# Performance work log

Measured on AMD Instinct MI355X. Metric: run time of the kernel, lower is better.

The kernel has to match this reference:

```python
import jax, jax.numpy as jnp
import numpy as np


def setup_inputs() -> dict:
    key = jax.random.key(0)
    ks = jax.random.split(key, 7)
    T, B, D, H, Q = 256, 128, 1024, 2048, 1024
    return {
        "x": jax.random.normal(ks[0], (T, B, D), dtype=jnp.float32),
        "h0": jax.random.normal(ks[1], (B, H), dtype=jnp.float32) * 0.01,
        "W_xh": jax.random.normal(ks[2], (D, H), dtype=jnp.float32) * 0.01,
        "W_hh": jax.random.normal(ks[3], (H, H), dtype=jnp.float32) * 0.01,
        "b_h": jnp.zeros((H,), dtype=jnp.float32),
        "W_hq": jax.random.normal(ks[4], (H, Q), dtype=jnp.float32) * 0.01,
        "b_q": jnp.zeros((Q,), dtype=jnp.float32),
    }


def reference(x, h0, W_xh, W_hh, b_h, W_hq, b_q):
    # x: (T, B, D); vanilla RNN recurrence with ReLU, per-step output projection.
    def step(h, xt):
        h = jax.nn.relu(xt @ W_xh + h @ W_hh + b_h)  # (B, H)
        return h, h @ W_hq + b_q                      # (B, Q)

    h, outs = jax.lax.scan(step, h0, x)               # outs: (T, B, Q)
    out = outs.reshape(-1, outs.shape[-1])            # torch.cat along dim 0 -> (T*B, Q)
    return out, h
```

## Files before the change

kernel.cpp:

```cpp
#include <hip/hip_runtime.h>
#include <hip/hip_bf16.h>

typedef __bf16 bf16_t;
typedef bf16_t bf16x8 __attribute__((ext_vector_type(8)));
typedef bf16_t bf16x4 __attribute__((ext_vector_type(4)));
typedef bf16_t bf16x2 __attribute__((ext_vector_type(2)));
typedef float f32x4 __attribute__((ext_vector_type(4)));
typedef float f32x2 __attribute__((ext_vector_type(2)));

__device__ __forceinline__ void load_lds16(const bf16_t* g, bf16_t* l) {
  __builtin_amdgcn_global_load_lds(
      (const __attribute__((address_space(1))) unsigned int*)g,
      (__attribute__((address_space(3))) unsigned int*)l,
      16, 0, 0);
}

__global__ void conv_f32_bf16(const float* __restrict__ src,
                              bf16_t* __restrict__ dst, long n) {
  long i = ((long)blockIdx.x * blockDim.x + threadIdx.x) * 8;
  if (i + 7 >= n) return;
  float4 a = *(const float4*)(src + i);
  float4 b = *(const float4*)(src + i + 4);
  bf16x8 v;
  v[0] = (bf16_t)a.x; v[1] = (bf16_t)a.y; v[2] = (bf16_t)a.z; v[3] = (bf16_t)a.w;
  v[4] = (bf16_t)b.x; v[5] = (bf16_t)b.y; v[6] = (bf16_t)b.z; v[7] = (bf16_t)b.w;
  *(bf16x8*)(dst + i) = v;
}

__global__ void conv_bf16_f32(const bf16_t* __restrict__ src,
                              float* __restrict__ dst, long n) {
  long i = (long)blockIdx.x * blockDim.x + threadIdx.x;
  if (i >= n) return;
  dst[i] = (float)src[i];
}

__global__ void transpose_conv(const float* __restrict__ src,
                               bf16_t* __restrict__ dst, int Ksrc, int Nsrc) {
  __shared__ float tile[32][33];
  int n0 = blockIdx.x * 32, k0 = blockIdx.y * 32;
  int tx = threadIdx.x, ty = threadIdx.y;
#pragma unroll
  for (int i = 0; i < 32; i += 8)
    tile[ty + i][tx] = src[(long)(k0 + ty + i) * Nsrc + n0 + tx];
  __syncthreads();
#pragma unroll
  for (int i = 0; i < 32; i += 8)
    dst[(long)(n0 + ty + i) * Ksrc + k0 + tx] = (bf16_t)tile[tx][ty + i];
}

template <int STORE_MODE>
__global__ __launch_bounds__(256) void gemm_bt_128(
    const bf16_t* __restrict__ A, const bf16_t* __restrict__ Bt,
    const float* __restrict__ bias, void* __restrict__ Dout,
    int M, int N, int K) {
  __shared__ bf16_t As[128 * 32];
  __shared__ bf16_t Bs[128 * 32];
  const int tid = threadIdx.x;
  const int lane = tid & 63;
  const int w = tid >> 6;
  const int wr = w >> 1, wc = w & 1;
  const int m0 = blockIdx.y * 128, n0 = blockIdx.x * 128;

  f32x4 acc[4][4] = {};

  const int r0 = tid >> 2;
  const int kk = (tid & 3) * 8;
  const int fr = lane & 15;
  const int fk = (lane >> 4) * 8;

  for (int k0 = 0; k0 < K; k0 += 32) {
    load_lds16(A + (long)(m0 + r0) * K + k0 + kk, As + w * 512);
    load_lds16(A + (long)(m0 + 64 + r0) * K + k0 + kk, As + 2048 + w * 512);
    load_lds16(Bt + (long)(n0 + r0) * K + k0 + kk, Bs + w * 512);
    load_lds16(Bt + (long)(n0 + 64 + r0) * K + k0 + kk, Bs + 2048 + w * 512);
    asm volatile("s_waitcnt vmcnt(0)" ::: "memory");
    __syncthreads();

    bf16x8 af[4], bfx[4];
#pragma unroll
    for (int m = 0; m < 4; ++m)
      af[m] = *(const bf16x8*)&As[(wr * 64 + m * 16 + fr) * 32 + fk];
#pragma unroll
    for (int n = 0; n < 4; ++n)
      bfx[n] = *(const bf16x8*)&Bs[(wc * 64 + n * 16 + fr) * 32 + fk];
#pragma unroll
    for (int m = 0; m < 4; ++m)
#pragma unroll
      for (int n = 0; n < 4; ++n)
        acc[m][n] = __builtin_amdgcn_mfma_f32_16x16x32_bf16(af[m], bfx[n],
                                                            acc[m][n], 0, 0, 0);
    __syncthreads();
  }

  const int fq = lane >> 4;
#pragma unroll
  for (int m = 0; m < 4; ++m) {
#pragma unroll
    for (int n = 0; n < 4; ++n) {
      int col = n0 + wc * 64 + n * 16 + fr;
      float bv = bias[col];
#pragma unroll
      for (int r = 0; r < 4; ++r) {
        int row = m0 + wr * 64 + m * 16 + fq * 4 + r;
        float v = acc[m][n][r] + bv;
        if (STORE_MODE == 0)
          ((float*)Dout)[(long)row * N + col] = v;
        else
          ((bf16_t*)Dout)[(long)row * N + col] = (bf16_t)v;
      }
    }
  }
}

__device__ __forceinline__ void half_bar(unsigned int* c, unsigned int target,
                                         int lane) {
  if (lane == 0)
    __hip_atomic_fetch_add(c, 1u, __ATOMIC_RELEASE,
                           __HIP_MEMORY_SCOPE_WORKGROUP);
  unsigned int v;
  do {
    v = __hip_atomic_load(c, __ATOMIC_ACQUIRE, __HIP_MEMORY_SCOPE_WORKGROUP);
    if (v >= target) break;
    __builtin_amdgcn_s_sleep(1);
  } while (true);
}

__global__ __launch_bounds__(512, 1) void rnn_persistent8(
    const bf16_t* __restrict__ h0,
    bf16_t* __restrict__ Hbuf,
    const bf16_t* __restrict__ WhhT,
    unsigned int* __restrict__ flags) {
  __shared__ bf16_t Wlds[65536];
  __shared__ float sred[2][4][16 * 36];
  __shared__ unsigned int barc[2];

  const int tid = threadIdx.x, lane = tid & 63, w = tid >> 6;
  const int h = w >> 2;
  const int lw = w & 3;
  const int gid = blockIdx.x;
  const int p = (gid >> 1) & 3;
  const int n0idx = ((gid & 1) << 5) | (gid >> 3);
  const int chain = p + h * 4;
  const int m0 = chain * 16, n0 = n0idx * 32;
  const int H = 2048;
  const long BH = 128L * 2048;
  const int kb = lw * 512;
  const int fr = lane & 15, fg = lane >> 4;
  const int w64 = lw * 64;

  {
    const int scol = tid >> 4;
    const int sk16 = tid & 15;
    const bf16_t* gsrc = WhhT + (long)(n0 + scol) * H + sk16 * 8;
#pragma unroll 4
    for (int j = 0; j < 16; ++j) {
      bf16x8 v = *(const bf16x8*)(gsrc + j * 128);
      int k8 = sk16 + j * 16;
      *(bf16x8*)&Wlds[(k8 * 32 + scol) * 8] = v;
    }
  }
  if (tid < 2) barc[tid] = 0;
  __syncthreads();

  const int halftid = tid & 255;
  const int jj = halftid * 2;
  const int zrow = jj >> 5, zcol = jj & 31;
  const int sidx = zrow * 36 + zcol;

  unsigned int* myflag = flags + (((chain << 6) | n0idx) << 4);
  const unsigned int* pollflag =
      flags + (((chain << 6) | (lw * 16 + (lane & 15))) << 4);
  unsigned int* bc = &barc[h];

  for (int t = 0; t < 256; ++t) {
    const bf16_t* hp = (t == 0) ? h0 : Hbuf + (long)(t - 1) * BH;
    bf16_t* z = Hbuf + (long)t * BH;
    const long zoff = (long)(m0 + zrow) * H + n0 + zcol;

    float zvr;
    {
      const bf16_t* zp = z + zoff;
      asm volatile("global_load_dword %0, %1, off sc0 sc1"
                   : "=v"(zvr)
                   : "v"(zp)
                   : "memory");
    }

    if (t > 0) {
      unsigned int v;
      do {
        v = __hip_atomic_load(pollflag, __ATOMIC_RELAXED,
                              __HIP_MEMORY_SCOPE_AGENT);
        if (__all(v >= (unsigned int)t)) break;
        __builtin_amdgcn_s_sleep(1);
      } while (true);
    }

    const bf16_t* Ab = hp + (long)(m0 + fr) * H + kb + fg * 8;
    f32x4 a0, a1, a2, a3, a4, a5, a6, a7, a8, a9, a10, a11, a12, a13, a14, a15;
    asm volatile(
        "global_load_dwordx4 %0, %16, off sc0\n\t"
        "global_load_dwordx4 %1, %16, off offset:64 sc0\n\t"
        "global_load_dwordx4 %2, %16, off offset:128 sc0\n\t"
        "global_load_dwordx4 %3, %16, off offset:192 sc0\n\t"
        "global_load_dwordx4 %4, %16, off offset:256 sc0\n\t"
        "global_load_dwordx4 %5, %16, off offset:320 sc0\n\t"
        "global_load_dwordx4 %6, %16, off offset:384 sc0\n\t"
        "global_load_dwordx4 %7, %16, off offset:448 sc0\n\t"
        "global_load_dwordx4 %8, %16, off offset:512 sc0\n\t"
        "global_load_dwordx4 %9, %16, off offset:576 sc0\n\t"
        "global_load_dwordx4 %10, %16, off offset:640 sc0\n\t"
        "global_load_dwordx4 %11, %16, off offset:704 sc0\n\t"
        "global_load_dwordx4 %12, %16, off offset:768 sc0\n\t"
        "global_load_dwordx4 %13, %16, off offset:832 sc0\n\t"
        "global_load_dwordx4 %14, %16, off offset:896 sc0\n\t"
        "global_load_dwordx4 %15, %16, off offset:960 sc0\n\t"
        "s_waitcnt vmcnt(0)"
        : "=&v"(a0), "=&v"(a1), "=&v"(a2), "=&v"(a3), "=&v"(a4), "=&v"(a5),
          "=&v"(a6), "=&v"(a7), "=&v"(a8), "=&v"(a9), "=&v"(a10), "=&v"(a11),
          "=&v"(a12), "=&v"(a13), "=&v"(a14), "=&v"(a15)
        : "v"(Ab)
        : "memory");
    __builtin_amdgcn_sched_barrier(0);

    f32x4 acc0 = {}, acc1 = {};
#define STEPX(ks, A)                                                          \
  {                                                                           \
    bf16x8 w0 = *(const bf16x8*)&Wlds[((w64 + (ks) * 4 + fg) * 32 + fr) * 8]; \
    bf16x8 w1 =                                                               \
        *(const bf16x8*)&Wlds[((w64 + (ks) * 4 + fg) * 32 + 16 + fr) * 8];    \
    bf16x8 av = __builtin_bit_cast(bf16x8, A);                                \
    acc0 = __builtin_amdgcn_mfma_f32_16x16x32_bf16(av, w0, acc0, 0, 0, 0);    \
    acc1 = __builtin_amdgcn_mfma_f32_16x16x32_bf16(av, w1, acc1, 0, 0, 0);    \
  }
    STEPX(0, a0)   STEPX(1, a1)   STEPX(2, a2)   STEPX(3, a3)
    STEPX(4, a4)   STEPX(5, a5)   STEPX(6, a6)   STEPX(7, a7)
    STEPX(8, a8)   STEPX(9, a9)   STEPX(10, a10) STEPX(11, a11)
    STEPX(12, a12) STEPX(13, a13) STEPX(14, a14) STEPX(15, a15)
#undef STEPX

#pragma unroll
    for (int rr = 0; rr < 4; ++rr) {
      sred[h][lw][(fg * 4 + rr) * 36 + fr] = acc0[rr];
      sred[h][lw][(fg * 4 + rr) * 36 + 16 + fr] = acc1[rr];
    }
    half_bar(bc, (unsigned int)(2 * t + 1) * 4, lane);

    f32x2 r = *(const f32x2*)&sred[h][0][sidx];
    {
      f32x2 r1 = *(const f32x2*)&sred[h][1][sidx];
      f32x2 r2 = *(const f32x2*)&sred[h][2][sidx];
      f32x2 r3 = *(const f32x2*)&sred[h][3][sidx];
      r = r + r1 + r2 + r3;
    }
    bf16x2 zv = __builtin_bit_cast(bf16x2, zvr);
    bf16x2 o;
#pragma unroll
    for (int c2 = 0; c2 < 2; ++c2) {
      float v = r[c2] + (float)zv[c2];
      o[c2] = (bf16_t)(v > 0.f ? v : 0.f);
    }
    const bf16_t* zp = z + zoff;
    {
      float ov = __builtin_bit_cast(float, o);
      asm volatile("global_store_dword %0, %1, off sc0 sc1" ::"v"(zp),
                   "v"(ov)
                   : "memory");
    }
    asm volatile("s_waitcnt vmcnt(0)" ::: "memory");
    half_bar(bc, (unsigned int)(2 * t + 2) * 4, lane);
    if (halftid == 0)
      __hip_atomic_store(myflag, (unsigned int)(t + 1), __ATOMIC_RELAXED,
                         __HIP_MEMORY_SCOPE_AGENT);
    {
      float dummy;
      asm volatile("global_load_dword %0, %1, off sc0"
                   : "=&v"(dummy)
                   : "v"(zp)
                   : "memory");
    }
  }
}

extern "C" void kernel_launch(void* const* d_in, const int* in_sizes, int n_in,
                              void* d_out, int out_size, void* d_ws,
                              size_t ws_size, hipStream_t stream) {
  const float* x   = (const float*)d_in[0];
  const float* h0  = (const float*)d_in[1];
  const float* Wxh = (const float*)d_in[2];
  const float* Whh = (const float*)d_in[3];
  const float* bh  = (const float*)d_in[4];
  const float* Whq = (const float*)d_in[5];
  const float* bq  = (const float*)d_in[6];
  float* out = (float*)d_out;

  const int T = 256, B = 128, D = 1024, H = 2048, Q = 1024;
  const long MB = (long)T * B;

  char* ws = (char*)d_ws;
  unsigned int* flags = (unsigned int*)ws;  ws += 512 * 64;
  bf16_t* x_bf = (bf16_t*)ws;  ws += MB * D * 2;
  bf16_t* Hbuf = (bf16_t*)ws;  ws += MB * H * 2;
  bf16_t* h0bf = (bf16_t*)ws;  ws += (long)B * H * 2;
  bf16_t* WxhT = (bf16_t*)ws;  ws += (long)H * D * 2;
  bf16_t* WhhT = (bf16_t*)ws;  ws += (long)H * H * 2;
  bf16_t* WhqT = (bf16_t*)ws;  ws += (long)Q * H * 2;

  hipMemsetAsync(flags, 0, 512 * 64, stream);

  conv_f32_bf16<<<(int)(MB * D / 8 / 256), 256, 0, stream>>>(x, x_bf, MB * D);
  conv_f32_bf16<<<(int)((long)B * H / 8 / 256), 256, 0, stream>>>(h0, h0bf,
                                                                  (long)B * H);
  transpose_conv<<<dim3(H / 32, D / 32), dim3(32, 8), 0, stream>>>(Wxh, WxhT, D, H);
  transpose_conv<<<dim3(H / 32, H / 32), dim3(32, 8), 0, stream>>>(Whh, WhhT, H, H);
  transpose_conv<<<dim3(Q / 32, H / 32), dim3(32, 8), 0, stream>>>(Whq, WhqT, H, Q);

  gemm_bt_128<1><<<dim3(H / 128, MB / 128), 256, 0, stream>>>(
      x_bf, WxhT, bh, Hbuf, (int)MB, H, D);

  rnn_persistent8<<<256, 512, 0, stream>>>(h0bf, Hbuf, WhhT, flags);

  gemm_bt_128<0><<<dim3(Q / 128, MB / 128), 256, 0, stream>>>(
      Hbuf, WhqT, bq, out, (int)MB, Q, H);

  conv_bf16_f32<<<(int)((long)B * H / 256), 256, 0, stream>>>(
      Hbuf + (long)(T - 1) * B * H, out + MB * Q, (long)B * H);
}
```

Measured before the change: 1.841 ms.

## Cut per-step barriers in persistent RNN kernel; single-wave epilogue with free flag

Replaces the two half-block barriers per timestep with one barrier plus an LDS 'free' flag. One wave per half now does the reduction, ReLU, 16-byte store and global flag publish, so the other waves can start the next step's load and MFMA work without waiting for the epilogue. Also drops the trailing dummy load, staggers the two halves at start, and switches the cross-block poll to an escalating sleep backoff. The backoff may add latency when a dependency arrives just after a long sleep, and putting the whole epilogue on a single wave lengthens that wave's critical path.

```diff
diff --git a/kernel.cpp b/kernel.cpp
--- a/kernel.cpp
+++ b/kernel.cpp
@@ -125,7 +125,7 @@
   } while (true);
 }
 
-__global__ __launch_bounds__(512, 1) void rnn_persistent8(
+__global__ __launch_bounds__(512, 1) void rnn_persistent10(
     const bf16_t* __restrict__ h0,
     bf16_t* __restrict__ Hbuf,
     const bf16_t* __restrict__ WhhT,
@@ -133,6 +133,7 @@
   __shared__ bf16_t Wlds[65536];
   __shared__ float sred[2][4][16 * 36];
   __shared__ unsigned int barc[2];
+  __shared__ unsigned int sfree[2];
 
   const int tid = threadIdx.x, lane = tid & 63, w = tid >> 6;
   const int h = w >> 2;
@@ -159,41 +160,58 @@
       *(bf16x8*)&Wlds[(k8 * 32 + scol) * 8] = v;
     }
   }
-  if (tid < 2) barc[tid] = 0;
+  if (tid < 2) { barc[tid] = 0; sfree[tid] = 0; }
   __syncthreads();
 
-  const int halftid = tid & 255;
-  const int jj = halftid * 2;
-  const int zrow = jj >> 5, zcol = jj & 31;
-  const int sidx = zrow * 36 + zcol;
+  if (h == 1) __builtin_amdgcn_s_sleep(64);
+
+  const int zrowW = lane >> 2, zcolW = (lane & 3) * 8;
+  const int sidx = zrowW * 36 + zcolW;
+  const long zoffW = (long)(m0 + zrowW) * H + n0 + zcolW;
 
   unsigned int* myflag = flags + (((chain << 6) | n0idx) << 4);
   const unsigned int* pollflag =
       flags + (((chain << 6) | (lw * 16 + (lane & 15))) << 4);
   unsigned int* bc = &barc[h];
+  unsigned int* sf = &sfree[h];
 
   for (int t = 0; t < 256; ++t) {
     const bf16_t* hp = (t == 0) ? h0 : Hbuf + (long)(t - 1) * BH;
     bf16_t* z = Hbuf + (long)t * BH;
-    const long zoff = (long)(m0 + zrow) * H + n0 + zcol;
-
-    float zvr;
-    {
-      const bf16_t* zp = z + zoff;
-      asm volatile("global_load_dword %0, %1, off sc0 sc1"
+
+    f32x4 zvr;
+    if (lw == 0) {
+      const bf16_t* zp = z + zoffW;
+      asm volatile("global_load_dwordx4 %0, %1, off sc0 sc1"
                    : "=v"(zvr)
                    : "v"(zp)
                    : "memory");
     }
 
     if (t > 0) {
-      unsigned int v;
-      do {
+      const unsigned int tt = (unsigned int)t;
+      unsigned int v = __hip_atomic_load(pollflag, __ATOMIC_RELAXED,
+                                         __HIP_MEMORY_SCOPE_AGENT);
+      if (!__all(v >= tt)) {
+        __builtin_amdgcn_s_sleep(2);
         v = __hip_atomic_load(pollflag, __ATOMIC_RELAXED,
                               __HIP_MEMORY_SCOPE_AGENT);
-        if (__all(v >= (unsigned int)t)) break;
-        __builtin_amdgcn_s_sleep(1);
-      } while (true);
+        if (!__all(v >= tt)) {
+          __builtin_amdgcn_s_sleep(4);
+          v = __hip_atomic_load(pollflag, __ATOMIC_RELAXED,
+                                __HIP_MEMORY_SCOPE_AGENT);
+          if (!__all(v >= tt)) {
+            __builtin_amdgcn_s_sleep(8);
+            v = __hip_atomic_load(pollflag, __ATOMIC_RELAXED,
+                                  __HIP_MEMORY_SCOPE_AGENT);
+            while (!__all(v >= tt)) {
+              __builtin_amdgcn_s_sleep(16);
+              v = __hip_atomic_load(pollflag, __ATOMIC_RELAXED,
+                                    __HIP_MEMORY_SCOPE_AGENT);
+            }
+          }
+        }
+      }
     }
 
     const bf16_t* Ab = hp + (long)(m0 + fr) * H + kb + fg * 8;
@@ -239,45 +257,51 @@
     STEPX(12, a12) STEPX(13, a13) STEPX(14, a14) STEPX(15, a15)
 #undef STEPX
 
+    if (t > 0) {
+      while (__hip_atomic_load(sf, __ATOMIC_ACQUIRE,
+                               __HIP_MEMORY_SCOPE_WORKGROUP) <
+             (unsigned int)t)
+        __builtin_amdgcn_s_sleep(1);
+    }
+
 #pragma unroll
     for (int rr = 0; rr < 4; ++rr) {
       sred[h][lw][(fg * 4 + rr) * 36 + fr] = acc0[rr];
       sred[h][lw][(fg * 4 + rr) * 36 + 16 + fr] = acc1[rr];
     }
-    half_bar(bc, (unsigned int)(2 * t + 1) * 4, lane);
-
-    f32x2 r = *(const f32x2*)&sred[h][0][sidx];
-    {
-      f32x2 r1 = *(const f32x2*)&sred[h][1][sidx];
-      f32x2 r2 = *(const f32x2*)&sred[h][2][sidx];
-      f32x2 r3 = *(const f32x2*)&sred[h][3][sidx];
-      r = r + r1 + r2 + r3;
-    }
-    bf16x2 zv = __builtin_bit_cast(bf16x2, zvr);
-    bf16x2 o;
-#pragma unroll
-    for (int c2 = 0; c2 < 2; ++c2) {
-      float v = r[c2] + (float)zv[c2];
-      o[c2] = (bf16_t)(v > 0.f ? v : 0.f);
-    }
-    const bf16_t* zp = z + zoff;
-    {
-      float ov = __builtin_bit_cast(float, o);
-      asm volatile("global_store_dword %0, %1, off sc0 sc1" ::"v"(zp),
-                   "v"(ov)
-                   : "memory");
-    }
-    asm volatile("s_waitcnt vmcnt(0)" ::: "memory");
-    half_bar(bc, (unsigned int)(2 * t + 2) * 4, lane);
-    if (halftid == 0)
-      __hip_atomic_store(myflag, (unsigned int)(t + 1), __ATOMIC_RELAXED,
-                         __HIP_MEMORY_SCOPE_AGENT);
-    {
-      float dummy;
-      asm volatile("global_load_dword %0, %1, off sc0"
-                   : "=&v"(dummy)
-                   : "v"(zp)
-                   : "memory");
+    half_bar(bc, (unsigned int)(t + 1) * 4, lane);
+
+    if (lw == 0) {
+      f32x4 slo = *(const f32x4*)&sred[h][0][sidx];
+      f32x4 shi = *(const f32x4*)&sred[h][0][sidx + 4];
+#pragma unroll
+      for (int ww = 1; ww < 4; ++ww) {
+        slo = slo + *(const f32x4*)&sred[h][ww][sidx];
+        shi = shi + *(const f32x4*)&sred[h][ww][sidx + 4];
+      }
+      bf16x8 zv = __builtin_bit_cast(bf16x8, zvr);
+      bf16x8 o;
+#pragma unroll
+      for (int c = 0; c < 4; ++c) {
+        float v0 = slo[c] + (float)zv[c];
+        float v1 = shi[c] + (float)zv[c + 4];
+        o[c] = (bf16_t)(v0 > 0.f ? v0 : 0.f);
+        o[c + 4] = (bf16_t)(v1 > 0.f ? v1 : 0.f);
+      }
+      const bf16_t* zp = z + zoffW;
+      {
+        f32x4 ov = __builtin_bit_cast(f32x4, o);
+        asm volatile("global_store_dwordx4 %0, %1, off sc0 sc1" ::"v"(zp),
+                     "v"(ov)
+                     : "memory");
+      }
+      asm volatile("s_waitcnt vmcnt(0)" ::: "memory");
+      if (lane == 0) {
+        __hip_atomic_store(myflag, (unsigned int)(t + 1), __ATOMIC_RELAXED,
+                           __HIP_MEMORY_SCOPE_AGENT);
+        __hip_atomic_store(sf, (unsigned int)(t + 1), __ATOMIC_RELEASE,
+                           __HIP_MEMORY_SCOPE_WORKGROUP);
+      }
     }
   }
 }
@@ -318,7 +342,7 @@
   gemm_bt_128<1><<<dim3(H / 128, MB / 128), 256, 0, stream>>>(
       x_bf, WxhT, bh, Hbuf, (int)MB, H, D);
 
-  rnn_persistent8<<<256, 512, 0, stream>>>(h0bf, Hbuf, WhhT, flags);
+  rnn_persistent10<<<256, 512, 0, stream>>>(h0bf, Hbuf, WhhT, flags);
 
   gemm_bt_128<0><<<dim3(Q / 128, MB / 128), 256, 0, stream>>>(
       Hbuf, WhqT, bq, out, (int)MB, Q, H);
```

Measured after the change: 1.762 ms. 1.04x faster.
